# Performance work log

Measured on AMD Instinct MI355X. Metric: run time of the kernel, lower is better.

Reference implementation:

```python
import jax, jax.numpy as jnp
import numpy as np

# Model dims (match init_kwargs)
D_MODEL = 512
N_LAYERS = 4
N_DIST = 32
N_CAT = 32
LATENT = N_DIST * N_CAT  # 1024
D_INNER = 2 * D_MODEL    # 1024 (mamba expand=2)
D_STATE = 16
DT_RANK = D_MODEL // 16  # 32
K = 4                    # depthwise conv kernel
BATCH, SEQ = 4, 1024


def setup_inputs() -> dict:
    key = jax.random.key(0)
    ks = jax.random.split(key, 12)
    f = lambda k, shape, s=0.02: (jax.random.normal(k, shape, jnp.float32) * s)
    inp = {
        "x": jax.random.normal(ks[0], (BATCH, SEQ, LATENT), jnp.float32),
        "lin1_w": f(ks[1], (LATENT, D_MODEL)),
        "lin1_b": jnp.zeros((D_MODEL,), jnp.float32),
        "norm_w": jnp.ones((N_LAYERS, D_MODEL), jnp.float32),
        "in_w": f(ks[2], (N_LAYERS, D_MODEL, 2 * D_INNER)),
        "conv_w": f(ks[3], (N_LAYERS, D_INNER, K), 0.1),
        "conv_b": jnp.zeros((N_LAYERS, D_INNER), jnp.float32),
        "xproj_w": f(ks[4], (N_LAYERS, D_INNER, DT_RANK + 2 * D_STATE)),
        "dt_w": f(ks[5], (N_LAYERS, DT_RANK, D_INNER)),
        "dt_b": f(ks[6], (N_LAYERS, D_INNER), 0.5),
        "A_log": jnp.log(jnp.broadcast_to(
            jnp.arange(1, D_STATE + 1, dtype=jnp.float32),
            (N_LAYERS, D_INNER, D_STATE))),
        "Dp": jnp.ones((N_LAYERS, D_INNER), jnp.float32),
        "out_w": f(ks[7], (N_LAYERS, D_INNER, D_MODEL)),
        "lin2_w": f(ks[8], (D_MODEL, LATENT)),
        "lin2_b": jnp.zeros((LATENT,), jnp.float32),
    }
    return inp


def _rmsnorm(x, w):
    return x * jax.lax.rsqrt(jnp.mean(x * x, axis=-1, keepdims=True) + 1e-5) * w


def _causal_dwconv(x, w, b):
    # x: (B,S,D), w: (D,K) -> depthwise causal conv1d, left-padded
    S = x.shape[1]
    xp = jnp.pad(x, ((0, 0), (K - 1, 0), (0, 0)))
    y = xp[:, 0:S, :] * w[:, 0]
    for k in range(1, K):
        y = y + xp[:, k:k + S, :] * w[:, k]
    return y + b


def _selective_scan(u, dt, Bm, Cm, A, Dvec):
    # u, dt: (B,S,D); Bm, Cm: (B,S,N); A: (D,N); Dvec: (D,)
    dA = jnp.exp(dt[..., None] * A)                               # (B,S,D,N)
    dBu = dt[..., None] * Bm[:, :, None, :] * u[..., None]        # (B,S,D,N)
    h0 = jnp.zeros((u.shape[0], u.shape[2], A.shape[1]), u.dtype)

    def step(h, inputs):
        dA_t, dBu_t, C_t = inputs
        h = dA_t * h + dBu_t                                       # (B,D,N)
        y = jnp.einsum('bdn,bn->bd', h, C_t)
        return h, y

    _, ys = jax.lax.scan(step, h0,
                         (dA.transpose(1, 0, 2, 3),
                          dBu.transpose(1, 0, 2, 3),
                          Cm.transpose(1, 0, 2)))
    return ys.transpose(1, 0, 2) + u * Dvec                       # (B,S,D)


def reference(x, lin1_w, lin1_b, norm_w, in_w, conv_w, conv_b, xproj_w,
              dt_w, dt_b, A_log, Dp, out_w, lin2_w, lin2_b):
    B, S, _ = x.shape
    h = x @ lin1_w + lin1_b                                       # (B,S,d_model)
    for l in range(N_LAYERS):
        resid = h
        hn = _rmsnorm(h, norm_w[l])
        xz = hn @ in_w[l]                                         # (B,S,2*d_inner)
        xp, z = jnp.split(xz, 2, axis=-1)
        xp = jax.nn.silu(_causal_dwconv(xp, conv_w[l], conv_b[l]))
        dbl = xp @ xproj_w[l]                                     # (B,S,dt_rank+2N)
        dt = jax.nn.softplus(dbl[..., :DT_RANK] @ dt_w[l] + dt_b[l])
        Bm = dbl[..., DT_RANK:DT_RANK + D_STATE]
        Cm = dbl[..., DT_RANK + D_STATE:]
        A = -jnp.exp(A_log[l])                                    # (d_inner, N)
        y = _selective_scan(xp, dt, Bm, Cm, A, Dp[l])
        y = y * jax.nn.silu(z)
        h = resid + y @ out_w[l]
    out = h @ lin2_w + lin2_b                                     # (B,S,latent)
    out = jax.nn.softmax(out.reshape(B, S, N_DIST, N_CAT), axis=-1)
    return out.reshape(B, S, N_DIST * N_CAT)
```

## Files before the change

### kernel.cpp

```cpp
#include <hip/hip_runtime.h>
#include <math.h>

#define D_MODEL 512
#define N_LAYERS 4
#define LATENT 1024
#define D_INNER 1024
#define D_STATE 16
#define DT_RANK 32
#define KCONV 4
#define BATCH 4
#define SEQ 1024
#define NTOK (BATCH * SEQ)
#define PCH 32
#define CLEN 32
#define NCAT 1152

typedef __attribute__((ext_vector_type(8))) short short8;
typedef __attribute__((ext_vector_type(4))) float floatx4;
typedef unsigned short ushort_t;

#define WC_VM4   0x0F74
#define WC_VM0   0x0F70
#define WC_LGKM0 0xC07F

__device__ __forceinline__ ushort_t f2bf(float f) {
    union { float f; unsigned u; } v; v.f = f;
    unsigned r = v.u + 0x7FFFu + ((v.u >> 16) & 1u);
    return (ushort_t)(r >> 16);
}
__device__ __forceinline__ float bf2f(ushort_t u) {
    union { unsigned u; float f; } v; v.u = ((unsigned)u) << 16;
    return v.f;
}
__device__ __forceinline__ void gll16(const void* g, void* l) {
    __builtin_amdgcn_global_load_lds(
        (const __attribute__((address_space(1))) void*)g,
        (__attribute__((address_space(3))) void*)l, 16, 0, 0);
}

__global__ __launch_bounds__(256, 3) void gemm_bf16_tile(
    const ushort_t* __restrict__ A, int lda,
    const ushort_t* __restrict__ Bt, int ldb,
    float* __restrict__ C, ushort_t* __restrict__ Cb, int ldc,
    const float* __restrict__ bias,
    int M, int N, int K, int flags)
{
    __shared__ ushort_t As[3][4096];
    __shared__ ushort_t Bs[3][4096];

    const int gx = gridDim.x;
    const int nwg = gx * gridDim.y;
    const int orig = blockIdx.y * gx + blockIdx.x;
    const int qq = nwg >> 3, rr = nwg & 7;
    const int xcd = orig & 7, loc = orig >> 3;
    const int swz = (xcd < rr ? xcd * (qq + 1) : rr * (qq + 1) + (xcd - rr) * qq) + loc;
    const int m0 = (swz / gx) * 64;
    const int n0 = (swz % gx) * 64;

    const int tid = threadIdx.x;
    const int w = tid >> 6;
    const int lane = tid & 63;
    const int quad = lane >> 4;
    const int l16 = lane & 15;
    const int wm = (w & 1) * 32;
    const int wn = (w >> 1) * 32;

    const int srow = tid >> 3;
    const int schunk = ((tid & 7) ^ (srow & 7)) * 8;
    const ushort_t* ga = A + (size_t)(m0 + srow) * lda + schunk;
    const ushort_t* gb = Bt + (size_t)(n0 + srow) * ldb + schunk;
    const int lofs = tid * 8;

    const int swz0 = ((0 * 4 + quad) ^ (l16 & 7)) * 8;
    const int swz1 = ((1 * 4 + quad) ^ (l16 & 7)) * 8;

    floatx4 acc[2][2] = {};
    const int nt = K >> 6;

    #define STAGE(t, b)                                         \
        do {                                                    \
            const ushort_t* pa_ = ga + (t) * 64;                \
            const ushort_t* pb_ = gb + (t) * 64;                \
            gll16(pa_, &As[(b)][lofs]);                         \
            gll16(pa_ + (size_t)32 * lda, &As[(b)][2048 + lofs]); \
            gll16(pb_, &Bs[(b)][lofs]);                         \
            gll16(pb_ + (size_t)32 * ldb, &Bs[(b)][2048 + lofs]); \
        } while (0)

    STAGE(0, 0);
    if (nt > 1) STAGE(1, 1);

    int cur = 0;
    for (int kt = 0; kt < nt; kt++) {
        if (kt + 1 < nt) __builtin_amdgcn_s_waitcnt(WC_VM4);
        else             __builtin_amdgcn_s_waitcnt(WC_VM0);
        __builtin_amdgcn_s_barrier();
        __builtin_amdgcn_sched_barrier(0);

        if (kt + 2 < nt) {
            int nb = cur + 2; if (nb >= 3) nb -= 3;
            STAGE(kt + 2, nb);
        }

        short8 af[2][2], bfr[2][2];
        #pragma unroll
        for (int i = 0; i < 2; i++) {
            const int r = wm + i * 16 + l16;
            af[0][i] = *(const short8*)&As[cur][r * 64 + swz0];
            af[1][i] = *(const short8*)&As[cur][r * 64 + swz1];
        }
        #pragma unroll
        for (int j = 0; j < 2; j++) {
            const int r = wn + j * 16 + l16;
            bfr[0][j] = *(const short8*)&Bs[cur][r * 64 + swz0];
            bfr[1][j] = *(const short8*)&Bs[cur][r * 64 + swz1];
        }
        __builtin_amdgcn_s_waitcnt(WC_LGKM0);
        __builtin_amdgcn_sched_barrier(0);

        #pragma unroll
        for (int ks = 0; ks < 2; ks++)
            #pragma unroll
            for (int i = 0; i < 2; i++)
                #pragma unroll
                for (int j = 0; j < 2; j++)
                    acc[i][j] = __builtin_amdgcn_mfma_f32_16x16x32_bf16(
                        af[ks][i], bfr[ks][j], acc[i][j], 0, 0, 0);

        cur++; if (cur == 3) cur = 0;
    }
    #undef STAGE

    #pragma unroll
    for (int j = 0; j < 2; j++) {
        int n = n0 + wn + j * 16 + l16;
        float bv = (flags & 1) ? bias[n] : 0.f;
        bool do_sp = (flags & 4) && (n < 1024);
        float spb = do_sp ? bias[n] : 0.f;
        #pragma unroll
        for (int i = 0; i < 2; i++) {
            int mrow = m0 + wm + i * 16 + quad * 4;
            #pragma unroll
            for (int rr2 = 0; rr2 < 4; rr2++) {
                size_t idx = (size_t)(mrow + rr2) * ldc + n;
                float v = acc[i][j][rr2] + bv;
                if (do_sp) {
                    v += spb;
                    v = (v > 20.f) ? v : log1pf(__expf(v));
                }
                if (flags & 8) {
                    Cb[idx] = f2bf(v);
                } else {
                    if (flags & 2) v += C[idx];
                    C[idx] = v;
                }
            }
        }
    }
}

__global__ __launch_bounds__(256) void build_wdt_kernel(
    const float* __restrict__ xproj_w, const float* __restrict__ dt_w,
    ushort_t* __restrict__ wcat)
{
    const int l = blockIdx.z;
    const int n0 = blockIdx.x * 64;
    const int k0 = blockIdx.y * 64;
    const float* xw  = xproj_w + (size_t)l * D_INNER * 64;
    const float* dtw = dt_w + (size_t)l * DT_RANK * D_INNER;

    __shared__ float xs[64][33];
    __shared__ float ds[32][65];

    const int tid = threadIdx.x;
    {
        int row = tid >> 2;
        int col = (tid & 3) * 8;
        #pragma unroll
        for (int q = 0; q < 8; q++)
            xs[row][col + q] = xw[(size_t)(k0 + row) * 64 + col + q];
    }
    {
        int row = tid >> 3;
        int col = (tid & 7) * 8;
        #pragma unroll
        for (int q = 0; q < 8; q++)
            ds[row][col + q] = dtw[(size_t)row * D_INNER + n0 + col + q];
    }
    __syncthreads();

    const int ty = tid & 15;
    const int tx = tid >> 4;
    float acc[4][4] = {};
    #pragma unroll
    for (int r = 0; r < 32; r++) {
        float a[4], b[4];
        #pragma unroll
        for (int i = 0; i < 4; i++) a[i] = xs[ty * 4 + i][r];
        #pragma unroll
        for (int j = 0; j < 4; j++) b[j] = ds[r][tx * 4 + j];
        #pragma unroll
        for (int j = 0; j < 4; j++)
            #pragma unroll
            for (int i = 0; i < 4; i++)
                acc[j][i] = fmaf(a[i], b[j], acc[j][i]);
    }
    #pragma unroll
    for (int j = 0; j < 4; j++) {
        int n = n0 + tx * 4 + j;
        ushort4 o;
        o.x = f2bf(acc[j][0]); o.y = f2bf(acc[j][1]);
        o.z = f2bf(acc[j][2]); o.w = f2bf(acc[j][3]);
        *(ushort4*)&wcat[((size_t)l * NCAT + n) * D_INNER + k0 + ty * 4] = o;
    }
}

__global__ __launch_bounds__(256) void build_wbc_kernel(
    const float* __restrict__ xproj_w, ushort_t* __restrict__ wcat)
{
    const int idx = blockIdx.x * 256 + threadIdx.x;
    const int k = idx & 1023;
    const int j = (idx >> 10) & 127;
    const int l = idx >> 17;
    ushort_t v = 0;
    if (j < 32)
        v = f2bf(xproj_w[((size_t)l * D_INNER + k) * 64 + 32 + j]);
    wcat[((size_t)l * NCAT + 1024 + j) * D_INNER + k] = v;
}

__global__ __launch_bounds__(256) void transpose_cast_kernel(
    const float* __restrict__ in, ushort_t* __restrict__ out, int K, int N)
{
    __shared__ float tile[32][33];
    const int n0 = blockIdx.x * 32, k0 = blockIdx.y * 32;
    const int tx = threadIdx.x & 31, ty = threadIdx.x >> 5;
    #pragma unroll
    for (int i = 0; i < 4; i++)
        tile[ty + i * 8][tx] = in[(size_t)(k0 + ty + i * 8) * N + n0 + tx];
    __syncthreads();
    #pragma unroll
    for (int i = 0; i < 4; i++)
        out[(size_t)(n0 + ty + i * 8) * K + k0 + tx] = f2bf(tile[tx][ty + i * 8]);
}

__global__ __launch_bounds__(256) void cast_bf16_kernel(
    const float* __restrict__ in, ushort_t* __restrict__ out)
{
    const int i = blockIdx.x * 256 + threadIdx.x;
    out[i] = f2bf(in[i]);
}

__global__ __launch_bounds__(256) void rmsnorm_kernel(
    const float* __restrict__ x, const float* __restrict__ w,
    ushort_t* __restrict__ y)
{
    const int row = blockIdx.x;
    const float* xr = x + (size_t)row * D_MODEL;
    ushort_t* yr = y + (size_t)row * D_MODEL;
    const int tid = threadIdx.x;

    float v0 = xr[tid], v1 = xr[tid + 256];
    float ss = v0 * v0 + v1 * v1;
    #pragma unroll
    for (int off = 32; off > 0; off >>= 1) ss += __shfl_down(ss, off);

    __shared__ float wsum[4];
    __shared__ float scale_s;
    int wid = tid >> 6, lane = tid & 63;
    if (lane == 0) wsum[wid] = ss;
    __syncthreads();
    if (tid == 0) {
        float tot = wsum[0] + wsum[1] + wsum[2] + wsum[3];
        scale_s = 1.0f / sqrtf(tot / (float)D_MODEL + 1e-5f);
    }
    __syncthreads();
    float sc = scale_s;
    yr[tid] = f2bf(v0 * sc * w[tid]);
    yr[tid + 256] = f2bf(v1 * sc * w[tid + 256]);
}

__global__ __launch_bounds__(256) void conv_silu_kernel(
    const ushort_t* __restrict__ xz, const float* __restrict__ w,
    const float* __restrict__ bconv, ushort_t* __restrict__ outb)
{
    const int idx = blockIdx.x * 256 + threadIdx.x;
    const int d = idx & (D_INNER - 1);
    const int t = (idx >> 10) & (SEQ - 1);
    const int row = idx >> 10;
    const ushort_t* base = xz + (size_t)row * 2048 + d;

    float s = 0.f;
    #pragma unroll
    for (int k = 0; k < KCONV; k++) {
        int tt = t + k - (KCONV - 1);
        if (tt >= 0)
            s = fmaf(bf2f(base[(ptrdiff_t)(k - (KCONV - 1)) * 2048]), w[d * KCONV + k], s);
    }
    s += bconv[d];
    float r = s / (1.f + __expf(-s));
    outb[idx] = f2bf(r);
}

__global__ __launch_bounds__(256) void scan_pass1(
    const float* __restrict__ dbl, const ushort_t* __restrict__ ub,
    const float* __restrict__ A_log,
    float* __restrict__ hfin, float* __restrict__ sumdt)
{
    const int tid = threadIdx.x;
    const int b = blockIdx.x >> 7;
    const int p = (blockIdx.x >> 2) & 31;
    const int d = ((blockIdx.x & 3) << 8) + tid;
    const int t0 = p * CLEN;

    float A[D_STATE];
    #pragma unroll
    for (int n = 0; n < D_STATE; n++) A[n] = -expf(A_log[d * D_STATE + n]);

    float h[D_STATE] = {};
    float sdt = 0.f;

    const float* dtp = dbl + ((size_t)b * SEQ + t0) * NCAT + d;
    const float* bp  = dbl + ((size_t)b * SEQ + t0) * NCAT + 1024;
    const ushort_t* up = ub + ((size_t)b * SEQ + t0) * D_INNER + d;

    for (int t = 0; t < CLEN; t++) {
        float dtv = dtp[(size_t)t * NCAT];
        float uv  = bf2f(up[(size_t)t * D_INNER]);
        float dtu = dtv * uv;
        sdt += dtv;
        #pragma unroll
        for (int n = 0; n < D_STATE; n++)
            h[n] = fmaf(__expf(dtv * A[n]), h[n], dtu * bp[t * NCAT + n]);
    }

    size_t base = (size_t)(b * PCH + p) * D_STATE * D_INNER + d;
    #pragma unroll
    for (int n = 0; n < D_STATE; n++) hfin[base + (size_t)n * D_INNER] = h[n];
    sumdt[(size_t)(b * PCH + p) * D_INNER + d] = sdt;
}

__global__ __launch_bounds__(256) void scan_pass2(
    const float* __restrict__ A_log, const float* __restrict__ sumdt,
    float* __restrict__ hc)
{
    const int tid = threadIdx.x;
    const int b = blockIdx.x >> 6;
    const int n = (blockIdx.x >> 2) & 15;
    const int d = ((blockIdx.x & 3) << 8) + tid;

    const float Aval = -expf(A_log[d * D_STATE + n]);
    float h = 0.f;
    for (int p = 0; p < PCH; p++) {
        size_t idx = ((size_t)(b * PCH + p) * D_STATE + n) * D_INNER + d;
        float fin = hc[idx];
        hc[idx] = h;
        h = fmaf(__expf(Aval * sumdt[(size_t)(b * PCH + p) * D_INNER + d]), h, fin);
    }
}

__global__ __launch_bounds__(256) void scan_pass3(
    const float* __restrict__ dbl, const ushort_t* __restrict__ xz,
    const float* __restrict__ A_log, const float* __restrict__ Dp,
    const float* __restrict__ hstart, ushort_t* ub)
{
    const int tid = threadIdx.x;
    const int b = blockIdx.x >> 7;
    const int p = (blockIdx.x >> 2) & 31;
    const int d = ((blockIdx.x & 3) << 8) + tid;
    const int t0 = p * CLEN;

    float A[D_STATE];
    #pragma unroll
    for (int n = 0; n < D_STATE; n++) A[n] = -expf(A_log[d * D_STATE + n]);
    const float Dv = Dp[d];

    float h[D_STATE];
    size_t base = (size_t)(b * PCH + p) * D_STATE * D_INNER + d;
    #pragma unroll
    for (int n = 0; n < D_STATE; n++) h[n] = hstart[base + (size_t)n * D_INNER];

    const float* dtp = dbl + ((size_t)b * SEQ + t0) * NCAT + d;
    const float* bp  = dbl + ((size_t)b * SEQ + t0) * NCAT + 1024;
    const ushort_t* zp = xz + ((size_t)b * SEQ + t0) * 2048 + 1024 + d;
    ushort_t* up = ub + ((size_t)b * SEQ + t0) * D_INNER + d;

    for (int t = 0; t < CLEN; t++) {
        float dtv = dtp[(size_t)t * NCAT];
        float uv  = bf2f(up[(size_t)t * D_INNER]);
        float zv  = bf2f(zp[(size_t)t * 2048]);
        float dtu = dtv * uv;
        float y = 0.f;
        #pragma unroll
        for (int n = 0; n < D_STATE; n++) {
            h[n] = fmaf(__expf(dtv * A[n]), h[n], dtu * bp[t * NCAT + n]);
            y = fmaf(h[n], bp[t * NCAT + 16 + n], y);
        }
        float res = fmaf(uv, Dv, y);
        res *= zv / (1.f + __expf(-zv));
        up[(size_t)t * D_INNER] = f2bf(res);
    }
}

__global__ __launch_bounds__(256) void softmax_kernel(
    const float* __restrict__ in, float* __restrict__ out)
{
    const int idx = blockIdx.x * 256 + threadIdx.x;
    float v = in[idx];
    float m = v;
    #pragma unroll
    for (int off = 16; off > 0; off >>= 1) m = fmaxf(m, __shfl_xor(m, off, 32));
    float e = expf(v - m);
    float s = e;
    #pragma unroll
    for (int off = 16; off > 0; off >>= 1) s += __shfl_xor(s, off, 32);
    out[idx] = e / s;
}

extern "C" void kernel_launch(void* const* d_in, const int* in_sizes, int n_in,
                              void* d_out, int out_size, void* d_ws, size_t ws_size,
                              hipStream_t stream)
{
    const float* x       = (const float*)d_in[0];
    const float* lin1_w  = (const float*)d_in[1];
    const float* lin1_b  = (const float*)d_in[2];
    const float* norm_w  = (const float*)d_in[3];
    const float* in_w    = (const float*)d_in[4];
    const float* conv_w  = (const float*)d_in[5];
    const float* conv_b  = (const float*)d_in[6];
    const float* xproj_w = (const float*)d_in[7];
    const float* dt_w    = (const float*)d_in[8];
    const float* dt_b    = (const float*)d_in[9];
    const float* A_log   = (const float*)d_in[10];
    const float* Dp      = (const float*)d_in[11];
    const float* out_w   = (const float*)d_in[12];
    const float* lin2_w  = (const float*)d_in[13];
    const float* lin2_b  = (const float*)d_in[14];
    float* outp = (float*)d_out;
    (void)ws_size; (void)in_sizes; (void)n_in; (void)out_size;

    float* ws = (float*)d_ws;
    const size_t F1M = 1u << 20;
    float* h     = ws;
    float* dbl   = h + 2 * F1M;
    float* sumdt = dbl + (size_t)NTOK * NCAT;
    float* hfin  = sumdt + (size_t)BATCH * PCH * D_INNER;
    ushort_t* xzb   = (ushort_t*)(hfin + 2 * F1M);
    ushort_t* hn_bf = xzb + 8 * F1M;
    ushort_t* xb    = hn_bf + 2 * F1M;
    ushort_t* lin1_wt = xb + 4 * F1M;
    ushort_t* in_wt   = lin1_wt + (size_t)512 * 1024;
    ushort_t* out_wt  = in_wt + (size_t)4 * 2048 * 512;
    ushort_t* lin2_wt = out_wt + (size_t)4 * 512 * 1024;
    ushort_t* wcat    = lin2_wt + (size_t)1024 * 512;

    dim3 blk(256);

    transpose_cast_kernel<<<dim3(512 / 32, 1024 / 32), blk, 0, stream>>>(
        lin1_w, lin1_wt, LATENT, D_MODEL);
    for (int l = 0; l < N_LAYERS; l++) {
        transpose_cast_kernel<<<dim3(2048 / 32, 512 / 32), blk, 0, stream>>>(
            in_w + (size_t)l * 512 * 2048, in_wt + (size_t)l * 2048 * 512, 512, 2048);
        transpose_cast_kernel<<<dim3(512 / 32, 1024 / 32), blk, 0, stream>>>(
            out_w + (size_t)l * 1024 * 512, out_wt + (size_t)l * 512 * 1024, 1024, 512);
    }
    transpose_cast_kernel<<<dim3(1024 / 32, 512 / 32), blk, 0, stream>>>(
        lin2_w, lin2_wt, D_MODEL, LATENT);
    build_wdt_kernel<<<dim3(16, 16, N_LAYERS), blk, 0, stream>>>(
        xproj_w, dt_w, wcat);
    build_wbc_kernel<<<dim3((N_LAYERS * 128 * 1024) / 256), blk, 0, stream>>>(
        xproj_w, wcat);

    cast_bf16_kernel<<<dim3((NTOK * LATENT) / 256), blk, 0, stream>>>(x, xb);

    gemm_bf16_tile<<<dim3(D_MODEL / 64, NTOK / 64), blk, 0, stream>>>(
        xb, LATENT, lin1_wt, LATENT, h, nullptr, D_MODEL, lin1_b,
        NTOK, D_MODEL, LATENT, 1);

    for (int l = 0; l < N_LAYERS; l++) {
        const float* nw = norm_w + (size_t)l * D_MODEL;
        const float* cw = conv_w + (size_t)l * D_INNER * KCONV;
        const float* cb = conv_b + (size_t)l * D_INNER;
        const float* db = dt_b + (size_t)l * D_INNER;
        const float* al = A_log + (size_t)l * D_INNER * D_STATE;
        const float* dp = Dp + (size_t)l * D_INNER;
        const ushort_t* iwt = in_wt + (size_t)l * 2048 * 512;
        const ushort_t* owt = out_wt + (size_t)l * 512 * 1024;
        const ushort_t* wc  = wcat + (size_t)l * NCAT * D_INNER;

        rmsnorm_kernel<<<dim3(NTOK), blk, 0, stream>>>(h, nw, hn_bf);

        gemm_bf16_tile<<<dim3(2048 / 64, NTOK / 64), blk, 0, stream>>>(
            hn_bf, D_MODEL, iwt, D_MODEL, nullptr, xzb, 2048, nullptr,
            NTOK, 2048, D_MODEL, 8);

        conv_silu_kernel<<<dim3((NTOK * D_INNER) / 256), blk, 0, stream>>>(
            xzb, cw, cb, xb);

        gemm_bf16_tile<<<dim3(NCAT / 64, NTOK / 64), blk, 0, stream>>>(
            xb, D_INNER, wc, D_INNER, dbl, nullptr, NCAT, db,
            NTOK, NCAT, D_INNER, 4);

        scan_pass1<<<dim3(BATCH * PCH * (D_INNER / 256)), blk, 0, stream>>>(
            dbl, xb, al, hfin, sumdt);
        scan_pass2<<<dim3(BATCH * D_STATE * (D_INNER / 256)), blk, 0, stream>>>(
            al, sumdt, hfin);
        scan_pass3<<<dim3(BATCH * PCH * (D_INNER / 256)), blk, 0, stream>>>(
            dbl, xzb, al, dp, hfin, xb);

        gemm_bf16_tile<<<dim3(D_MODEL / 64, NTOK / 64), blk, 0, stream>>>(
            xb, D_INNER, owt, D_INNER, h, nullptr, D_MODEL, nullptr,
            NTOK, D_MODEL, D_INNER, 2);
    }

    cast_bf16_kernel<<<dim3((NTOK * D_MODEL) / 256), blk, 0, stream>>>(h, xb);
    gemm_bf16_tile<<<dim3(LATENT / 64, NTOK / 64), blk, 0, stream>>>(
        xb, D_MODEL, lin2_wt, D_MODEL, dbl, nullptr, LATENT, lin2_b,
        NTOK, LATENT, D_MODEL, 1);
    softmax_kernel<<<dim3((NTOK * LATENT) / 256), blk, 0, stream>>>(dbl, outp);
}
```

Measured before the change: 782.8 us.

## Replace 4-wave GEMM tile with single-wave 64x64 tile kernel

The bf16 MFMA GEMM now runs each 64x64 output tile on one 64-thread wave instead of four waves. The single wave holds a 4x4 accumulator grid and loads all staging data itself, and the triple-buffered LDS pipeline becomes double-buffered. With one wave per block, workgroup barriers are no longer needed and each wave reuses its fragments across 16 MFMAs. The cost is more registers per wave, longer serial issue of global-to-LDS loads, and less latency hiding inside a tile, which must come from running more blocks per CU.

```diff
diff --git a/kernel.cpp b/kernel.cpp
--- a/kernel.cpp
+++ b/kernel.cpp
@@ -19,8 +19,8 @@
 typedef __attribute__((ext_vector_type(4))) float floatx4;
 typedef unsigned short ushort_t;
 
-#define WC_VM4   0x0F74
 #define WC_VM0   0x0F70
+#define WC_VM16  0x4F70
 #define WC_LGKM0 0xC07F
 
 __device__ __forceinline__ ushort_t f2bf(float f) {
@@ -38,15 +38,15 @@
         (__attribute__((address_space(3))) void*)l, 16, 0, 0);
 }
 
-__global__ __launch_bounds__(256, 3) void gemm_bf16_tile(
+__global__ __launch_bounds__(64) void gemm_bf16_wave(
     const ushort_t* __restrict__ A, int lda,
     const ushort_t* __restrict__ Bt, int ldb,
     float* __restrict__ C, ushort_t* __restrict__ Cb, int ldc,
     const float* __restrict__ bias,
     int M, int N, int K, int flags)
 {
-    __shared__ ushort_t As[3][4096];
-    __shared__ ushort_t Bs[3][4096];
+    __shared__ ushort_t As[2][4096];
+    __shared__ ushort_t Bs[2][4096];
 
     const int gx = gridDim.x;
     const int nwg = gx * gridDim.y;
@@ -57,89 +57,87 @@
     const int m0 = (swz / gx) * 64;
     const int n0 = (swz % gx) * 64;
 
-    const int tid = threadIdx.x;
-    const int w = tid >> 6;
-    const int lane = tid & 63;
+    const int lane = threadIdx.x;
     const int quad = lane >> 4;
     const int l16 = lane & 15;
-    const int wm = (w & 1) * 32;
-    const int wn = (w >> 1) * 32;
-
-    const int srow = tid >> 3;
-    const int schunk = ((tid & 7) ^ (srow & 7)) * 8;
+
+    const int srow = lane >> 3;
+    const int schunk = ((lane & 7) ^ srow) * 8;
     const ushort_t* ga = A + (size_t)(m0 + srow) * lda + schunk;
     const ushort_t* gb = Bt + (size_t)(n0 + srow) * ldb + schunk;
-    const int lofs = tid * 8;
+    const int lofs = lane * 8;
 
     const int swz0 = ((0 * 4 + quad) ^ (l16 & 7)) * 8;
     const int swz1 = ((1 * 4 + quad) ^ (l16 & 7)) * 8;
 
-    floatx4 acc[2][2] = {};
+    floatx4 acc[4][4] = {};
     const int nt = K >> 6;
 
-    #define STAGE(t, b)                                         \
-        do {                                                    \
-            const ushort_t* pa_ = ga + (t) * 64;                \
-            const ushort_t* pb_ = gb + (t) * 64;                \
-            gll16(pa_, &As[(b)][lofs]);                         \
-            gll16(pa_ + (size_t)32 * lda, &As[(b)][2048 + lofs]); \
-            gll16(pb_, &Bs[(b)][lofs]);                         \
-            gll16(pb_ + (size_t)32 * ldb, &Bs[(b)][2048 + lofs]); \
+    #define STAGE(t, b)                                                    \
+        do {                                                               \
+            const ushort_t* pa_ = ga + (t) * 64;                           \
+            const ushort_t* pb_ = gb + (t) * 64;                           \
+            _Pragma("unroll")                                              \
+            for (int q = 0; q < 8; q++) {                                  \
+                gll16(pa_ + (size_t)(q * 8) * lda, &As[(b)][q * 512 + lofs]); \
+                gll16(pb_ + (size_t)(q * 8) * ldb, &Bs[(b)][q * 512 + lofs]); \
+            }                                                              \
         } while (0)
 
     STAGE(0, 0);
-    if (nt > 1) STAGE(1, 1);
-
-    int cur = 0;
+
     for (int kt = 0; kt < nt; kt++) {
-        if (kt + 1 < nt) __builtin_amdgcn_s_waitcnt(WC_VM4);
-        else             __builtin_amdgcn_s_waitcnt(WC_VM0);
-        __builtin_amdgcn_s_barrier();
+        const int cur = kt & 1;
+        if (kt + 1 < nt) {
+            STAGE(kt + 1, cur ^ 1);
+            __builtin_amdgcn_s_waitcnt(WC_VM16);
+        } else {
+            __builtin_amdgcn_s_waitcnt(WC_VM0);
+        }
         __builtin_amdgcn_sched_barrier(0);
 
-        if (kt + 2 < nt) {
-            int nb = cur + 2; if (nb >= 3) nb -= 3;
-            STAGE(kt + 2, nb);
-        }
-
-        short8 af[2][2], bfr[2][2];
-        #pragma unroll
-        for (int i = 0; i < 2; i++) {
-            const int r = wm + i * 16 + l16;
-            af[0][i] = *(const short8*)&As[cur][r * 64 + swz0];
-            af[1][i] = *(const short8*)&As[cur][r * 64 + swz1];
-        }
-        #pragma unroll
-        for (int j = 0; j < 2; j++) {
-            const int r = wn + j * 16 + l16;
-            bfr[0][j] = *(const short8*)&Bs[cur][r * 64 + swz0];
-            bfr[1][j] = *(const short8*)&Bs[cur][r * 64 + swz1];
-        }
+        short8 af[4], bf[4];
+        #pragma unroll
+        for (int i = 0; i < 4; i++)
+            af[i] = *(const short8*)&As[cur][(i * 16 + l16) * 64 + swz0];
+        #pragma unroll
+        for (int j = 0; j < 4; j++)
+            bf[j] = *(const short8*)&Bs[cur][(j * 16 + l16) * 64 + swz0];
         __builtin_amdgcn_s_waitcnt(WC_LGKM0);
         __builtin_amdgcn_sched_barrier(0);
-
-        #pragma unroll
-        for (int ks = 0; ks < 2; ks++)
+        #pragma unroll
+        for (int i = 0; i < 4; i++)
             #pragma unroll
-            for (int i = 0; i < 2; i++)
-                #pragma unroll
-                for (int j = 0; j < 2; j++)
-                    acc[i][j] = __builtin_amdgcn_mfma_f32_16x16x32_bf16(
-                        af[ks][i], bfr[ks][j], acc[i][j], 0, 0, 0);
-
-        cur++; if (cur == 3) cur = 0;
+            for (int j = 0; j < 4; j++)
+                acc[i][j] = __builtin_amdgcn_mfma_f32_16x16x32_bf16(
+                    af[i], bf[j], acc[i][j], 0, 0, 0);
+
+        #pragma unroll
+        for (int i = 0; i < 4; i++)
+            af[i] = *(const short8*)&As[cur][(i * 16 + l16) * 64 + swz1];
+        #pragma unroll
+        for (int j = 0; j < 4; j++)
+            bf[j] = *(const short8*)&Bs[cur][(j * 16 + l16) * 64 + swz1];
+        __builtin_amdgcn_s_waitcnt(WC_LGKM0);
+        __builtin_amdgcn_sched_barrier(0);
+        #pragma unroll
+        for (int i = 0; i < 4; i++)
+            #pragma unroll
+            for (int j = 0; j < 4; j++)
+                acc[i][j] = __builtin_amdgcn_mfma_f32_16x16x32_bf16(
+                    af[i], bf[j], acc[i][j], 0, 0, 0);
     }
     #undef STAGE
 
     #pragma unroll
-    for (int j = 0; j < 2; j++) {
-        int n = n0 + wn + j * 16 + l16;
+    for (int j = 0; j < 4; j++) {
+        int n = n0 + j * 16 + l16;
         float bv = (flags & 1) ? bias[n] : 0.f;
         bool do_sp = (flags & 4) && (n < 1024);
         float spb = do_sp ? bias[n] : 0.f;
         #pragma unroll
-        for (int i = 0; i < 2; i++) {
-            int mrow = m0 + wm + i * 16 + quad * 4;
+        for (int i = 0; i < 4; i++) {
+            int mrow = m0 + i * 16 + quad * 4;
             #pragma unroll
             for (int rr2 = 0; rr2 < 4; rr2++) {
                 size_t idx = (size_t)(mrow + rr2) * ldc + n;
@@ -454,6 +452,7 @@
     ushort_t* wcat    = lin2_wt + (size_t)1024 * 512;
 
     dim3 blk(256);
+    dim3 wblk(64);
 
     transpose_cast_kernel<<<dim3(512 / 32, 1024 / 32), blk, 0, stream>>>(
         lin1_w, lin1_wt, LATENT, D_MODEL);
@@ -472,7 +471,7 @@
 
     cast_bf16_kernel<<<dim3((NTOK * LATENT) / 256), blk, 0, stream>>>(x, xb);
 
-    gemm_bf16_tile<<<dim3(D_MODEL / 64, NTOK / 64), blk, 0, stream>>>(
+    gemm_bf16_wave<<<dim3(D_MODEL / 64, NTOK / 64), wblk, 0, stream>>>(
         xb, LATENT, lin1_wt, LATENT, h, nullptr, D_MODEL, lin1_b,
         NTOK, D_MODEL, LATENT, 1);
 
@@ -489,14 +488,14 @@
 
         rmsnorm_kernel<<<dim3(NTOK), blk, 0, stream>>>(h, nw, hn_bf);
 
-        gemm_bf16_tile<<<dim3(2048 / 64, NTOK / 64), blk, 0, stream>>>(
+        gemm_bf16_wave<<<dim3(2048 / 64, NTOK / 64), wblk, 0, stream>>>(
             hn_bf, D_MODEL, iwt, D_MODEL, nullptr, xzb, 2048, nullptr,
             NTOK, 2048, D_MODEL, 8);
 
         conv_silu_kernel<<<dim3((NTOK * D_INNER) / 256), blk, 0, stream>>>(
             xzb, cw, cb, xb);
 
-        gemm_bf16_tile<<<dim3(NCAT / 64, NTOK / 64), blk, 0, stream>>>(
+        gemm_bf16_wave<<<dim3(NCAT / 64, NTOK / 64), wblk, 0, stream>>>(
             xb, D_INNER, wc, D_INNER, dbl, nullptr, NCAT, db,
             NTOK, NCAT, D_INNER, 4);
 
@@ -507,13 +506,13 @@
         scan_pass3<<<dim3(BATCH * PCH * (D_INNER / 256)), blk, 0, stream>>>(
             dbl, xzb, al, dp, hfin, xb);
 
-        gemm_bf16_tile<<<dim3(D_MODEL / 64, NTOK / 64), blk, 0, stream>>>(
+        gemm_bf16_wave<<<dim3(D_MODEL / 64, NTOK / 64), wblk, 0, stream>>>(
             xb, D_INNER, owt, D_INNER, h, nullptr, D_MODEL, nullptr,
             NTOK, D_MODEL, D_INNER, 2);
     }
 
     cast_bf16_kernel<<<dim3((NTOK * D_MODEL) / 256), blk, 0, stream>>>(h, xb);
-    gemm_bf16_tile<<<dim3(LATENT / 64, NTOK / 64), blk, 0, stream>>>(
+    gemm_bf16_wave<<<dim3(LATENT / 64, NTOK / 64), wblk, 0, stream>>>(
         xb, D_MODEL, lin2_wt, D_MODEL, dbl, nullptr, LATENT, lin2_b,
         NTOK, LATENT, D_MODEL, 1);
     softmax_kernel<<<dim3((NTOK * LATENT) / 256), blk, 0, stream>>>(dbl, outp);
```

Result: slower. 997.6 us (+27.4%).

## Split fused xproj-dt GEMM into two factored low-rank GEMMs

Applied to the files above, without the earlier changes.

The old code pre-multiplied xproj_w and dt_w into one 1152-wide weight, then ran a K=1024 GEMM per layer. The new code runs x@xproj_w (N=64, K=1024) and writes both fp32 and bf16 copies through a new epilogue flag. A second GEMM (K=64) then produces dt with softplus. This cuts GEMM FLOPs roughly tenfold for this stage but adds a launch, a small-grid GEMM with low occupancy, and a second bf16 rounding of the dt-rank intermediate.

```diff
diff --git a/kernel.cpp b/kernel.cpp
--- a/kernel.cpp
+++ b/kernel.cpp
@@ -13,7 +13,6 @@
 #define NTOK (BATCH * SEQ)
 #define PCH 32
 #define CLEN 32
-#define NCAT 1152
 
 typedef __attribute__((ext_vector_type(8))) short short8;
 typedef __attribute__((ext_vector_type(4))) float floatx4;
@@ -153,79 +152,24 @@
                 } else {
                     if (flags & 2) v += C[idx];
                     C[idx] = v;
+                    if (flags & 16) Cb[idx] = f2bf(v);
                 }
             }
         }
     }
 }
 
-__global__ __launch_bounds__(256) void build_wdt_kernel(
-    const float* __restrict__ xproj_w, const float* __restrict__ dt_w,
-    ushort_t* __restrict__ wcat)
-{
-    const int l = blockIdx.z;
-    const int n0 = blockIdx.x * 64;
-    const int k0 = blockIdx.y * 64;
-    const float* xw  = xproj_w + (size_t)l * D_INNER * 64;
-    const float* dtw = dt_w + (size_t)l * DT_RANK * D_INNER;
-
-    __shared__ float xs[64][33];
-    __shared__ float ds[32][65];
-
-    const int tid = threadIdx.x;
-    {
-        int row = tid >> 2;
-        int col = (tid & 3) * 8;
-        #pragma unroll
-        for (int q = 0; q < 8; q++)
-            xs[row][col + q] = xw[(size_t)(k0 + row) * 64 + col + q];
-    }
-    {
-        int row = tid >> 3;
-        int col = (tid & 7) * 8;
-        #pragma unroll
-        for (int q = 0; q < 8; q++)
-            ds[row][col + q] = dtw[(size_t)row * D_INNER + n0 + col + q];
-    }
-    __syncthreads();
-
-    const int ty = tid & 15;
-    const int tx = tid >> 4;
-    float acc[4][4] = {};
-    #pragma unroll
-    for (int r = 0; r < 32; r++) {
-        float a[4], b[4];
-        #pragma unroll
-        for (int i = 0; i < 4; i++) a[i] = xs[ty * 4 + i][r];
-        #pragma unroll
-        for (int j = 0; j < 4; j++) b[j] = ds[r][tx * 4 + j];
-        #pragma unroll
-        for (int j = 0; j < 4; j++)
-            #pragma unroll
-            for (int i = 0; i < 4; i++)
-                acc[j][i] = fmaf(a[i], b[j], acc[j][i]);
-    }
-    #pragma unroll
-    for (int j = 0; j < 4; j++) {
-        int n = n0 + tx * 4 + j;
-        ushort4 o;
-        o.x = f2bf(acc[j][0]); o.y = f2bf(acc[j][1]);
-        o.z = f2bf(acc[j][2]); o.w = f2bf(acc[j][3]);
-        *(ushort4*)&wcat[((size_t)l * NCAT + n) * D_INNER + k0 + ty * 4] = o;
-    }
-}
-
-__global__ __launch_bounds__(256) void build_wbc_kernel(
-    const float* __restrict__ xproj_w, ushort_t* __restrict__ wcat)
+__global__ __launch_bounds__(256) void build_w2t_kernel(
+    const float* __restrict__ dt_w, ushort_t* __restrict__ w2t)
 {
     const int idx = blockIdx.x * 256 + threadIdx.x;
-    const int k = idx & 1023;
-    const int j = (idx >> 10) & 127;
-    const int l = idx >> 17;
+    const int k = idx & 63;
+    const int n = (idx >> 6) & 1023;
+    const int l = idx >> 16;
     ushort_t v = 0;
-    if (j < 32)
-        v = f2bf(xproj_w[((size_t)l * D_INNER + k) * 64 + 32 + j]);
-    wcat[((size_t)l * NCAT + 1024 + j) * D_INNER + k] = v;
+    if (k < 32)
+        v = f2bf(dt_w[((size_t)l * DT_RANK + k) * D_INNER + n]);
+    w2t[((size_t)l * 1024 + n) * 64 + k] = v;
 }
 
 __global__ __launch_bounds__(256) void transpose_cast_kernel(
@@ -302,8 +246,8 @@
 }
 
 __global__ __launch_bounds__(256) void scan_pass1(
-    const float* __restrict__ dbl, const ushort_t* __restrict__ ub,
-    const float* __restrict__ A_log,
+    const float* __restrict__ dtb, const float* __restrict__ bc,
+    const ushort_t* __restrict__ ub, const float* __restrict__ A_log,
     float* __restrict__ hfin, float* __restrict__ sumdt)
 {
     const int tid = threadIdx.x;
@@ -319,18 +263,18 @@
     float h[D_STATE] = {};
     float sdt = 0.f;
 
-    const float* dtp = dbl + ((size_t)b * SEQ + t0) * NCAT + d;
-    const float* bp  = dbl + ((size_t)b * SEQ + t0) * NCAT + 1024;
+    const float* dtp = dtb + ((size_t)b * SEQ + t0) * 1024 + d;
+    const float* bp  = bc + ((size_t)b * SEQ + t0) * 64 + 32;
     const ushort_t* up = ub + ((size_t)b * SEQ + t0) * D_INNER + d;
 
     for (int t = 0; t < CLEN; t++) {
-        float dtv = dtp[(size_t)t * NCAT];
+        float dtv = dtp[(size_t)t * 1024];
         float uv  = bf2f(up[(size_t)t * D_INNER]);
         float dtu = dtv * uv;
         sdt += dtv;
         #pragma unroll
         for (int n = 0; n < D_STATE; n++)
-            h[n] = fmaf(__expf(dtv * A[n]), h[n], dtu * bp[t * NCAT + n]);
+            h[n] = fmaf(__expf(dtv * A[n]), h[n], dtu * bp[t * 64 + n]);
     }
 
     size_t base = (size_t)(b * PCH + p) * D_STATE * D_INNER + d;
@@ -359,9 +303,10 @@
 }
 
 __global__ __launch_bounds__(256) void scan_pass3(
-    const float* __restrict__ dbl, const ushort_t* __restrict__ xz,
-    const float* __restrict__ A_log, const float* __restrict__ Dp,
-    const float* __restrict__ hstart, ushort_t* ub)
+    const float* __restrict__ dtb, const float* __restrict__ bc,
+    const ushort_t* __restrict__ xz, const float* __restrict__ A_log,
+    const float* __restrict__ Dp, const float* __restrict__ hstart,
+    ushort_t* ub)
 {
     const int tid = threadIdx.x;
     const int b = blockIdx.x >> 7;
@@ -379,21 +324,21 @@
     #pragma unroll
     for (int n = 0; n < D_STATE; n++) h[n] = hstart[base + (size_t)n * D_INNER];
 
-    const float* dtp = dbl + ((size_t)b * SEQ + t0) * NCAT + d;
-    const float* bp  = dbl + ((size_t)b * SEQ + t0) * NCAT + 1024;
+    const float* dtp = dtb + ((size_t)b * SEQ + t0) * 1024 + d;
+    const float* bp  = bc + ((size_t)b * SEQ + t0) * 64 + 32;
     const ushort_t* zp = xz + ((size_t)b * SEQ + t0) * 2048 + 1024 + d;
     ushort_t* up = ub + ((size_t)b * SEQ + t0) * D_INNER + d;
 
     for (int t = 0; t < CLEN; t++) {
-        float dtv = dtp[(size_t)t * NCAT];
+        float dtv = dtp[(size_t)t * 1024];
         float uv  = bf2f(up[(size_t)t * D_INNER]);
         float zv  = bf2f(zp[(size_t)t * 2048]);
         float dtu = dtv * uv;
         float y = 0.f;
         #pragma unroll
         for (int n = 0; n < D_STATE; n++) {
-            h[n] = fmaf(__expf(dtv * A[n]), h[n], dtu * bp[t * NCAT + n]);
-            y = fmaf(h[n], bp[t * NCAT + 16 + n], y);
+            h[n] = fmaf(__expf(dtv * A[n]), h[n], dtu * bp[t * 64 + n]);
+            y = fmaf(h[n], bp[t * 64 + 16 + n], y);
         }
         float res = fmaf(uv, Dv, y);
         res *= zv / (1.f + __expf(-zv));
@@ -441,17 +386,20 @@
     float* ws = (float*)d_ws;
     const size_t F1M = 1u << 20;
     float* h     = ws;
-    float* dbl   = h + 2 * F1M;
-    float* sumdt = dbl + (size_t)NTOK * NCAT;
+    float* dtb   = h + 2 * F1M;
+    float* dblr  = dtb + 4 * F1M;
+    float* sumdt = dblr + (size_t)NTOK * 64;
     float* hfin  = sumdt + (size_t)BATCH * PCH * D_INNER;
-    ushort_t* xzb   = (ushort_t*)(hfin + 2 * F1M);
-    ushort_t* hn_bf = xzb + 8 * F1M;
-    ushort_t* xb    = hn_bf + 2 * F1M;
-    ushort_t* lin1_wt = xb + 4 * F1M;
+    ushort_t* xzb     = (ushort_t*)(hfin + 2 * F1M);
+    ushort_t* hn_bf   = xzb + 8 * F1M;
+    ushort_t* xb      = hn_bf + 2 * F1M;
+    ushort_t* dblr_bf = xb + 4 * F1M;
+    ushort_t* lin1_wt = dblr_bf + (size_t)NTOK * 64;
     ushort_t* in_wt   = lin1_wt + (size_t)512 * 1024;
     ushort_t* out_wt  = in_wt + (size_t)4 * 2048 * 512;
     ushort_t* lin2_wt = out_wt + (size_t)4 * 512 * 1024;
-    ushort_t* wcat    = lin2_wt + (size_t)1024 * 512;
+    ushort_t* xw_t    = lin2_wt + (size_t)1024 * 512;
+    ushort_t* w2t     = xw_t + (size_t)4 * 64 * 1024;
 
     dim3 blk(256);
 
@@ -462,13 +410,13 @@
             in_w + (size_t)l * 512 * 2048, in_wt + (size_t)l * 2048 * 512, 512, 2048);
         transpose_cast_kernel<<<dim3(512 / 32, 1024 / 32), blk, 0, stream>>>(
             out_w + (size_t)l * 1024 * 512, out_wt + (size_t)l * 512 * 1024, 1024, 512);
+        transpose_cast_kernel<<<dim3(64 / 32, 1024 / 32), blk, 0, stream>>>(
+            xproj_w + (size_t)l * D_INNER * 64, xw_t + (size_t)l * 64 * 1024, 1024, 64);
     }
     transpose_cast_kernel<<<dim3(1024 / 32, 512 / 32), blk, 0, stream>>>(
         lin2_w, lin2_wt, D_MODEL, LATENT);
-    build_wdt_kernel<<<dim3(16, 16, N_LAYERS), blk, 0, stream>>>(
-        xproj_w, dt_w, wcat);
-    build_wbc_kernel<<<dim3((N_LAYERS * 128 * 1024) / 256), blk, 0, stream>>>(
-        xproj_w, wcat);
+    build_w2t_kernel<<<dim3((N_LAYERS * 1024 * 64) / 256), blk, 0, stream>>>(
+        dt_w, w2t);
 
     cast_bf16_kernel<<<dim3((NTOK * LATENT) / 256), blk, 0, stream>>>(x, xb);
 
@@ -485,7 +433,8 @@
         const float* dp = Dp + (size_t)l * D_INNER;
         const ushort_t* iwt = in_wt + (size_t)l * 2048 * 512;
         const ushort_t* owt = out_wt + (size_t)l * 512 * 1024;
-        const ushort_t* wc  = wcat + (size_t)l * NCAT * D_INNER;
+        const ushort_t* xwt = xw_t + (size_t)l * 64 * 1024;
+        const ushort_t* w2  = w2t + (size_t)l * 1024 * 64;
 
         rmsnorm_kernel<<<dim3(NTOK), blk, 0, stream>>>(h, nw, hn_bf);
 
@@ -496,16 +445,20 @@
         conv_silu_kernel<<<dim3((NTOK * D_INNER) / 256), blk, 0, stream>>>(
             xzb, cw, cb, xb);
 
-        gemm_bf16_tile<<<dim3(NCAT / 64, NTOK / 64), blk, 0, stream>>>(
-            xb, D_INNER, wc, D_INNER, dbl, nullptr, NCAT, db,
-            NTOK, NCAT, D_INNER, 4);
+        gemm_bf16_tile<<<dim3(64 / 64, NTOK / 64), blk, 0, stream>>>(
+            xb, D_INNER, xwt, D_INNER, dblr, dblr_bf, 64, nullptr,
+            NTOK, 64, D_INNER, 16);
+
+        gemm_bf16_tile<<<dim3(1024 / 64, NTOK / 64), blk, 0, stream>>>(
+            dblr_bf, 64, w2, 64, dtb, nullptr, 1024, db,
+            NTOK, 1024, 64, 4);
 
         scan_pass1<<<dim3(BATCH * PCH * (D_INNER / 256)), blk, 0, stream>>>(
-            dbl, xb, al, hfin, sumdt);
+            dtb, dblr, xb, al, hfin, sumdt);
         scan_pass2<<<dim3(BATCH * D_STATE * (D_INNER / 256)), blk, 0, stream>>>(
             al, sumdt, hfin);
         scan_pass3<<<dim3(BATCH * PCH * (D_INNER / 256)), blk, 0, stream>>>(
-            dbl, xzb, al, dp, hfin, xb);
+            dtb, dblr, xzb, al, dp, hfin, xb);
 
         gemm_bf16_tile<<<dim3(D_MODEL / 64, NTOK / 64), blk, 0, stream>>>(
             xb, D_INNER, owt, D_INNER, h, nullptr, D_MODEL, nullptr,
@@ -514,7 +467,7 @@
 
     cast_bf16_kernel<<<dim3((NTOK * D_MODEL) / 256), blk, 0, stream>>>(h, xb);
     gemm_bf16_tile<<<dim3(LATENT / 64, NTOK / 64), blk, 0, stream>>>(
-        xb, D_MODEL, lin2_wt, D_MODEL, dbl, nullptr, LATENT, lin2_b,
+        xb, D_MODEL, lin2_wt, D_MODEL, dtb, nullptr, LATENT, lin2_b,
         NTOK, LATENT, D_MODEL, 1);
-    softmax_kernel<<<dim3((NTOK * LATENT) / 256), blk, 0, stream>>>(dbl, outp);
-}
+    softmax_kernel<<<dim3((NTOK * LATENT) / 256), blk, 0, stream>>>(dtb, outp);
+}
```

Result: faster. 756.8 us (-3.3%).
